# Kernel optimization log

Hardware: AMD Instinct MI355X
Metric: run time of the kernel (lower is better)

Reference implementation:

```python
import jax, jax.numpy as jnp
import numpy as np

B, N = 2048, 4095  # batch, number of spherical points (cumsum length = N+1)


def setup_inputs() -> dict:
    key = jax.random.key(0)
    k1, k2, k3, k4, k5 = jax.random.split(key, 5)
    return {
        "origin_3D": jax.random.uniform(k1, (B, 3, 1), dtype=jnp.float32),
        "spherical_3D": jax.random.uniform(k2, (B, 3, N), dtype=jnp.float32),
        "origin_2D": jax.random.uniform(k3, (B, 3, 1), dtype=jnp.float32),
        "spherical_2D": jax.random.uniform(k4, (B, 3, N), dtype=jnp.float32),
        "deformation_field": jax.random.uniform(k5, (B, 2, N), dtype=jnp.float32),
    }


def _cart(origin, spherical):
    # spherical: [B, 3, N] with rows (r, theta, phi)
    r, theta, phi = spherical[:, 0, :], spherical[:, 1, :], spherical[:, 2, :]
    st = jnp.sin(theta)
    x = r * st * jnp.cos(phi)
    y = r * st * jnp.sin(phi)
    z = r * jnp.cos(theta)
    shape = jnp.stack((x, y, z), axis=1)            # [B, 3, N]
    full = jnp.concatenate((origin, shape), axis=2)  # [B, 3, N+1]
    # torch.matmul(full, triu(ones)) == prefix sum along the last axis
    return jnp.cumsum(full, axis=2)


def reference(origin_3D, spherical_3D, origin_2D, spherical_2D, deformation_field):
    spherical_3D_deformed = spherical_3D.at[:, 1:, :].add(deformation_field)
    original_cart = _cart(origin_2D, spherical_2D)            # [B, 3, N+1]
    deformed_cart = _cart(origin_3D, spherical_3D_deformed)   # [B, 3, N+1]
    per_pt = jnp.sum(jnp.abs(deformed_cart - original_cart), axis=1)  # [B, N+1]
    return jnp.sum(jnp.mean(per_pt, axis=1))  # scalar
```

## Files before the change

### kernel.cpp

```cpp
#include <hip/hip_runtime.h>


#define BATCH 2048
#define NPTS  4095
#define POS   4096
#define T     1024
#define NW    16
#define CH    4

typedef float f4 __attribute__((ext_vector_type(4), aligned(4)));

__device__ __forceinline__ void sincos_poly(float x, float* s, float* c) {
    const float x2 = x * x;
    float ps = 2.7557319e-6f;
    ps = fmaf(ps, x2, -1.9841270e-4f);
    ps = fmaf(ps, x2,  8.3333333e-3f);
    ps = fmaf(ps, x2, -1.6666667e-1f);
    ps = fmaf(ps, x2,  1.0f);
    *s = x * ps;
    float pc = -2.7557319e-7f;
    pc = fmaf(pc, x2,  2.4801587e-5f);
    pc = fmaf(pc, x2, -1.3888889e-3f);
    pc = fmaf(pc, x2,  4.1666667e-2f);
    pc = fmaf(pc, x2, -0.5f);
    pc = fmaf(pc, x2,  1.0f);
    *c = pc;
}

__launch_bounds__(T, 4)
__global__ void mpd_loss_kernel(const float* __restrict__ origin3,
                                const float* __restrict__ sph3,
                                const float* __restrict__ origin2,
                                const float* __restrict__ sph2,
                                const float* __restrict__ def,
                                float* __restrict__ bsum) {
    __shared__ float wtot[3][NW];
    __shared__ float wsum[NW];

    const int b    = blockIdx.x;
    const int t    = threadIdx.x;
    const int lane = t & 63;
    const int w    = t >> 6;
    const bool lastT = (t == T - 1);

    const float* r3  = sph3 + (size_t)b * 3 * NPTS;
    const float* th3 = r3 + NPTS;
    const float* ph3 = th3 + NPTS;
    const float* r2  = sph2 + (size_t)b * 3 * NPTS;
    const float* th2 = r2 + NPTS;
    const float* ph2 = th2 + NPTS;
    const float* d0  = def + (size_t)b * 2 * NPTS;
    const float* d1  = d0 + NPTS;

    const int n0 = lastT ? (NPTS - CH) : (t * CH);

    const f4 vR3 = *(const f4*)(r3  + n0);
    const f4 vT3 = *(const f4*)(th3 + n0);
    const f4 vP3 = *(const f4*)(ph3 + n0);
    const f4 vR2 = *(const f4*)(r2  + n0);
    const f4 vT2 = *(const f4*)(th2 + n0);
    const f4 vP2 = *(const f4*)(ph2 + n0);
    const f4 vD0 = *(const f4*)(d0  + n0);
    const f4 vD1 = *(const f4*)(d1  + n0);

    float dx[CH], dy[CH], dz[CH];
    float tx = 0.f, ty = 0.f, tz = 0.f;
    #pragma unroll
    for (int k = 0; k < CH; ++k) {
        const bool valid = !(lastT && k == 0);
        const float R3  = vR3[k];
        const float Th3 = vT3[k] + vD0[k];
        const float Ph3 = vP3[k] + vD1[k];
        const float R2  = vR2[k];
        const float Th2 = vT2[k];
        const float Ph2 = vP2[k];
        float s3, c3, sp3, cp3, s2, c2, sp2, cp2;
        sincos_poly(Th3, &s3, &c3);
        sincos_poly(Ph3, &sp3, &cp3);
        sincos_poly(Th2, &s2, &c2);
        sincos_poly(Ph2, &sp2, &cp2);
        const float rs3 = R3 * s3;
        const float rs2 = R2 * s2;
        float ddx = rs3 * cp3 - rs2 * cp2;
        float ddy = rs3 * sp3 - rs2 * sp2;
        float ddz = R3 * c3 - R2 * c2;
        if (!valid) { ddx = 0.f; ddy = 0.f; ddz = 0.f; }
        dx[k] = ddx; dy[k] = ddy; dz[k] = ddz;
        tx += ddx; ty += ddy; tz += ddz;
    }

    float ix = tx, iy = ty, iz = tz;
    #pragma unroll
    for (int off = 1; off < 64; off <<= 1) {
        const float ux = __shfl_up(ix, off, 64);
        const float uy = __shfl_up(iy, off, 64);
        const float uz = __shfl_up(iz, off, 64);
        if (lane >= off) { ix += ux; iy += uy; iz += uz; }
    }
    if (lane == 63) { wtot[0][w] = ix; wtot[1][w] = iy; wtot[2][w] = iz; }
    __syncthreads();

    float wox = 0.f, woy = 0.f, woz = 0.f;
    #pragma unroll
    for (int ww = 0; ww < NW; ++ww) {
        if (ww < w) { wox += wtot[0][ww]; woy += wtot[1][ww]; woz += wtot[2][ww]; }
    }

    const float* o3 = origin3 + (size_t)b * 3;
    const float* o2 = origin2 + (size_t)b * 3;
    const float odx = o3[0] - o2[0];
    const float ody = o3[1] - o2[1];
    const float odz = o3[2] - o2[2];

    float px = odx + wox + (ix - tx);
    float py = ody + woy + (iy - ty);
    float pz = odz + woz + (iz - tz);
    float acc = (t == 0) ? (fabsf(odx) + fabsf(ody) + fabsf(odz)) : 0.f;
    #pragma unroll
    for (int k = 0; k < CH; ++k) {
        const bool valid = !(lastT && k == 0);
        px += dx[k]; py += dy[k]; pz += dz[k];
        if (valid) acc += fabsf(px) + fabsf(py) + fabsf(pz);
    }

    #pragma unroll
    for (int off = 32; off > 0; off >>= 1) acc += __shfl_down(acc, off, 64);
    if (lane == 0) wsum[w] = acc;
    __syncthreads();
    if (t == 0) {
        float s = 0.f;
        #pragma unroll
        for (int i = 0; i < NW; ++i) s += wsum[i];
        bsum[b] = s * (1.0f / POS);
    }
}

__launch_bounds__(256)
__global__ void reduce_kernel(const float* __restrict__ bsum, float* __restrict__ out) {
    const int t = threadIdx.x;
    float acc = 0.f;
    #pragma unroll
    for (int i = 0; i < BATCH / 256; ++i) acc += bsum[t + i * 256];
    #pragma unroll
    for (int off = 32; off > 0; off >>= 1) acc += __shfl_down(acc, off, 64);
    __shared__ float wred[4];
    if ((t & 63) == 0) wred[t >> 6] = acc;
    __syncthreads();
    if (t == 0) out[0] = wred[0] + wred[1] + wred[2] + wred[3];
}

extern "C" void kernel_launch(void* const* d_in, const int* in_sizes, int n_in,
                              void* d_out, int out_size, void* d_ws, size_t ws_size,
                              hipStream_t stream) {
    const float* origin3 = (const float*)d_in[0];
    const float* sph3    = (const float*)d_in[1];
    const float* origin2 = (const float*)d_in[2];
    const float* sph2    = (const float*)d_in[3];
    const float* def     = (const float*)d_in[4];
    float* out  = (float*)d_out;
    float* bsum = (float*)d_ws;

    mpd_loss_kernel<<<BATCH, T, 0, stream>>>(origin3, sph3, origin2, sph2, def, bsum);
    reduce_kernel<<<1, 256, 0, stream>>>(bsum, out);
}
```

Before: 264.8 us.

## Use 256-thread blocks with 16 points per thread and double-buffered loads

Shrinks the block from 1024 to 256 threads so each thread processes 16 points instead of 4. The points are handled in four chunks of 4, with the next chunk's vector loads issued, and pinned by an empty asm barrier, before the current chunk is computed, so load latency overlaps the sincos arithmetic. Running prefix values are kept per point, which reduces the scan and sync work per point. In exchange it raises register pressure from two sets of loaded vectors plus 48 prefix floats, and each block has fewer waves to hide latency.

```diff
diff --git a/kernel.cpp b/kernel.cpp
--- a/kernel.cpp
+++ b/kernel.cpp
@@ -4,9 +4,10 @@
 #define BATCH 2048
 #define NPTS  4095
 #define POS   4096
-#define T     1024
-#define NW    16
-#define CH    4
+#define T     256
+#define NW    4
+#define CH    16
+#define CK    4
 
 typedef float f4 __attribute__((ext_vector_type(4), aligned(4)));
 
@@ -26,6 +27,49 @@
     pc = fmaf(pc, x2,  1.0f);
     *c = pc;
 }
+
+template<int CBASE, bool MASK0>
+__device__ __forceinline__ void comp4(const f4 R3v, const f4 T3v, const f4 P3v,
+                                      const f4 R2v, const f4 T2v, const f4 P2v,
+                                      const f4 D0v, const f4 D1v,
+                                      bool lastT,
+                                      float (&px)[CH], float (&py)[CH], float (&pz)[CH],
+                                      float& rx, float& ry, float& rz) {
+    #pragma unroll
+    for (int k = 0; k < CK; ++k) {
+        const float R3  = R3v[k];
+        const float Th3 = T3v[k] + D0v[k];
+        const float Ph3 = P3v[k] + D1v[k];
+        const float R2  = R2v[k];
+        const float Th2 = T2v[k];
+        const float Ph2 = P2v[k];
+        float s3, c3, sp3, cp3, s2, c2, sp2, cp2;
+        sincos_poly(Th3, &s3, &c3);
+        sincos_poly(Ph3, &sp3, &cp3);
+        sincos_poly(Th2, &s2, &c2);
+        sincos_poly(Ph2, &sp2, &cp2);
+        const float rs3 = R3 * s3;
+        const float rs2 = R2 * s2;
+        float ddx = rs3 * cp3 - rs2 * cp2;
+        float ddy = rs3 * sp3 - rs2 * sp2;
+        float ddz = R3 * c3 - R2 * c2;
+        if (MASK0 && k == 0 && lastT) { ddx = 0.f; ddy = 0.f; ddz = 0.f; }
+        rx += ddx; ry += ddy; rz += ddz;
+        px[CBASE + k] = rx; py[CBASE + k] = ry; pz[CBASE + k] = rz;
+    }
+}
+
+#define LOADP(s, off)                                                        \
+    s##R3 = *(const f4*)(r3  + (off));                                       \
+    s##T3 = *(const f4*)(th3 + (off));                                       \
+    s##P3 = *(const f4*)(ph3 + (off));                                       \
+    s##R2 = *(const f4*)(r2  + (off));                                       \
+    s##T2 = *(const f4*)(th2 + (off));                                       \
+    s##P2 = *(const f4*)(ph2 + (off));                                       \
+    s##D0 = *(const f4*)(d0  + (off));                                       \
+    s##D1 = *(const f4*)(d1  + (off));                                       \
+    asm volatile("" : "+v"(s##R3), "+v"(s##T3), "+v"(s##P3), "+v"(s##R2),    \
+                      "+v"(s##T2), "+v"(s##P2), "+v"(s##D0), "+v"(s##D1));
 
 __launch_bounds__(T, 4)
 __global__ void mpd_loss_kernel(const float* __restrict__ origin3,
@@ -54,40 +98,22 @@
 
     const int n0 = lastT ? (NPTS - CH) : (t * CH);
 
-    const f4 vR3 = *(const f4*)(r3  + n0);
-    const f4 vT3 = *(const f4*)(th3 + n0);
-    const f4 vP3 = *(const f4*)(ph3 + n0);
-    const f4 vR2 = *(const f4*)(r2  + n0);
-    const f4 vT2 = *(const f4*)(th2 + n0);
-    const f4 vP2 = *(const f4*)(ph2 + n0);
-    const f4 vD0 = *(const f4*)(d0  + n0);
-    const f4 vD1 = *(const f4*)(d1  + n0);
+    f4 aR3, aT3, aP3, aR2, aT2, aP2, aD0, aD1;
+    f4 nR3, nT3, nP3, nR2, nT2, nP2, nD0, nD1;
 
-    float dx[CH], dy[CH], dz[CH];
-    float tx = 0.f, ty = 0.f, tz = 0.f;
-    #pragma unroll
-    for (int k = 0; k < CH; ++k) {
-        const bool valid = !(lastT && k == 0);
-        const float R3  = vR3[k];
-        const float Th3 = vT3[k] + vD0[k];
-        const float Ph3 = vP3[k] + vD1[k];
-        const float R2  = vR2[k];
-        const float Th2 = vT2[k];
-        const float Ph2 = vP2[k];
-        float s3, c3, sp3, cp3, s2, c2, sp2, cp2;
-        sincos_poly(Th3, &s3, &c3);
-        sincos_poly(Ph3, &sp3, &cp3);
-        sincos_poly(Th2, &s2, &c2);
-        sincos_poly(Ph2, &sp2, &cp2);
-        const float rs3 = R3 * s3;
-        const float rs2 = R2 * s2;
-        float ddx = rs3 * cp3 - rs2 * cp2;
-        float ddy = rs3 * sp3 - rs2 * sp2;
-        float ddz = R3 * c3 - R2 * c2;
-        if (!valid) { ddx = 0.f; ddy = 0.f; ddz = 0.f; }
-        dx[k] = ddx; dy[k] = ddy; dz[k] = ddz;
-        tx += ddx; ty += ddy; tz += ddz;
-    }
+    float px[CH], py[CH], pz[CH];
+    float rx = 0.f, ry = 0.f, rz = 0.f;
+
+    LOADP(a, n0)
+    LOADP(n, n0 + 4)
+    comp4<0, true >(aR3, aT3, aP3, aR2, aT2, aP2, aD0, aD1, lastT, px, py, pz, rx, ry, rz);
+    LOADP(a, n0 + 8)
+    comp4<4, false>(nR3, nT3, nP3, nR2, nT2, nP2, nD0, nD1, lastT, px, py, pz, rx, ry, rz);
+    LOADP(n, n0 + 12)
+    comp4<8, false>(aR3, aT3, aP3, aR2, aT2, aP2, aD0, aD1, lastT, px, py, pz, rx, ry, rz);
+    comp4<12, false>(nR3, nT3, nP3, nR2, nT2, nP2, nD0, nD1, lastT, px, py, pz, rx, ry, rz);
+
+    const float tx = rx, ty = ry, tz = rz;
 
     float ix = tx, iy = ty, iz = tz;
     #pragma unroll
@@ -112,15 +138,15 @@
     const float ody = o3[1] - o2[1];
     const float odz = o3[2] - o2[2];
 
-    float px = odx + wox + (ix - tx);
-    float py = ody + woy + (iy - ty);
-    float pz = odz + woz + (iz - tz);
+    const float ox = odx + wox + (ix - tx);
+    const float oy = ody + woy + (iy - ty);
+    const float oz = odz + woz + (iz - tz);
+
     float acc = (t == 0) ? (fabsf(odx) + fabsf(ody) + fabsf(odz)) : 0.f;
     #pragma unroll
     for (int k = 0; k < CH; ++k) {
         const bool valid = !(lastT && k == 0);
-        px += dx[k]; py += dy[k]; pz += dz[k];
-        if (valid) acc += fabsf(px) + fabsf(py) + fabsf(pz);
+        if (valid) acc += fabsf(px[k] + ox) + fabsf(py[k] + oy) + fabsf(pz[k] + oz);
     }
 
     #pragma unroll
```

Result: slower. 295.8 us (+11.7%).
